# Performance work log

Hardware: AMD Instinct MI355X
Metric: run time of the kernel (lower is better)

Reference implementation:

```python
import jax, jax.numpy as jnp
import numpy as np
import math

N, E = 10000, 160000
MUL0, MUL1 = 64, 32        # node irreps: 64x0e + 32x1o (dim 160)
M0, M1 = 32, 16            # msg irreps: 32x0e + 16x1o (dim 80)
H = 8                      # attention heads
NB = 16                    # radial basis size
C0 = M0 + M1               # coupled scalar mul (48)
C1 = M0 + M1 + M1          # coupled vector mul (64)
WNUM = M0 + M1 + M0 + M1 + M1  # uvu tensor-product weight numel (112)
EPS = 1e-5
SCALE = 1.0 / math.sqrt(M0 + M1)  # 1/sqrt(num_irreps of msg)
MDIM = M0 + 3 * M1


def o3_linear(x0, x1, W0, W1):
    # e3nn o3.Linear: mixes multiplicities within each degree l, shared over m,
    # with 1/sqrt(fan_in) path normalization.
    y0 = (x0 @ W0) * (1.0 / math.sqrt(x0.shape[-1]))
    y1 = jnp.einsum('euc,uv->evc', x1, W1) * (1.0 / math.sqrt(x1.shape[-2]))
    return y0, y1


def setup_inputs() -> dict:
    key = jax.random.key(0)
    k = jax.random.split(key, 16)
    node = jax.random.normal(k[0], (N, MUL0 + 3 * MUL1), jnp.float32)
    rbf = jax.random.normal(k[1], (E, NB), jnp.float32)
    d = jax.random.normal(k[2], (E, 3), jnp.float32)
    d = d / jnp.linalg.norm(d, axis=-1, keepdims=True)
    # component-normalized real spherical harmonics up to l=1: [1, sqrt(3)*r_hat]
    rsh = jnp.concatenate([jnp.ones((E, 1), jnp.float32), math.sqrt(3.0) * d], axis=-1)
    edge_index = jax.random.randint(k[3], (2, E), 0, N, dtype=jnp.int32)
    w = lambda i, shape: jax.random.normal(k[i], shape, jnp.float32)
    return dict(
        node=node, rbf=rbf, rsh=rsh, edge_index=edge_index,
        gamma0=jnp.ones((MUL0,), jnp.float32), gamma1=jnp.ones((MUL1,), jnp.float32),
        Wq0=w(4, (MUL0, H * M0)), Wq1=w(5, (MUL1, H * M1)),
        Wsrc0=w(6, (MUL0, M0)), Wsrc1=w(7, (MUL1, M1)),
        Wdst0=w(8, (MUL0, M0)), Wdst1=w(9, (MUL1, M1)),
        W_rbf=w(10, (NB, WNUM)),
        Wkv0=w(11, (C0, 2 * H * M0)), Wkv1=w(12, (C1, 2 * H * M1)),
        Wmsg0=w(13, (H * M0, MUL0)), Wmsg1=w(14, (H * M1, MUL1)),
    )


def reference(node, rbf, rsh, edge_index, gamma0, gamma1, Wq0, Wq1, Wsrc0, Wsrc1,
              Wdst0, Wdst1, W_rbf, Wkv0, Wkv1, Wmsg0, Wmsg1):
    n = node.shape[0]
    src_i, dst_i = edge_index[0], edge_index[1]
    n0 = node[:, :MUL0]
    n1 = node[:, MUL0:].reshape(n, MUL1, 3)
    # --- equivariant layer norm: standard LN on scalars, RMS-of-norms on vectors ---
    mu = n0.mean(-1, keepdims=True)
    var = ((n0 - mu) ** 2).mean(-1, keepdims=True)
    h0 = (n0 - mu) / jnp.sqrt(var + EPS) * gamma0
    vn = (n1 ** 2).sum(-1).mean(-1, keepdims=True)          # (n,1)
    h1 = n1 / jnp.sqrt(vn + EPS)[..., None] * gamma1[None, :, None]
    # --- query (per-head msg irreps layout) ---
    q0, q1 = o3_linear(h0, h1, Wq0, Wq1)
    q = jnp.concatenate([q0.reshape(n, H, M0),
                         q1.reshape(n, H, M1, 3).reshape(n, H, 3 * M1)], axis=-1)  # (n,H,MDIM)
    # --- per-edge src/dst features ---
    s0, s1 = o3_linear(h0, h1, Wsrc0, Wsrc1)
    d0, d1 = o3_linear(h0, h1, Wdst0, Wdst1)
    x0 = s0[src_i] + d0[dst_i]            # (E, M0)
    x1 = s1[src_i] + d1[dst_i]            # (E, M1, 3)
    # --- CG tensor product ('uvu', external per-edge weights from rbf) ---
    w = rbf @ W_rbf                       # (E, WNUM)
    o = np.cumsum([0, M0, M1, M0, M1, M1])
    w000 = w[:, o[0]:o[1]]; w110 = w[:, o[1]:o[2]]
    w011 = w[:, o[2]:o[3]]; w101 = w[:, o[3]:o[4]]; w111 = w[:, o[4]:o[5]]
    y0 = rsh[:, :1]                       # l=0 sh
    y1 = rsh[:, 1:]                       # l=1 sh
    c0a = w000 * x0 * y0                                                  # 0x0->0
    c0b = w110 * (x1 * y1[:, None, :]).sum(-1) * (1.0 / math.sqrt(3.0))   # 1x1->0
    c1a = w011[..., None] * x0[..., None] * y1[:, None, :]                # 0x1->1
    c1b = w101[..., None] * x1 * y0[..., None]                            # 1x0->1
    c1c = w111[..., None] * jnp.cross(x1, y1[:, None, :]) * (1.0 / math.sqrt(2.0))  # 1x1->1
    cp0 = jnp.concatenate([c0a, c0b], axis=-1)        # (E, C0)
    cp1 = jnp.concatenate([c1a, c1b, c1c], axis=1)    # (E, C1, 3)
    # --- key / value ---
    kv0, kv1 = o3_linear(cp0, cp1, Wkv0, Wkv1)
    kv = jnp.concatenate([kv0.reshape(-1, 2 * H, M0),
                          kv1.reshape(-1, 2 * H, M1, 3).reshape(-1, 2 * H, 3 * M1)], axis=-1)
    kkey, val = kv[:, :H], kv[:, H:]      # (E,H,MDIM) each
    # --- segment softmax over destination nodes (torch_geometric.utils.softmax) ---
    logits = (q[src_i] * kkey).sum(-1, keepdims=True) * SCALE   # (E,H,1)
    smax = jax.ops.segment_max(logits, dst_i, num_segments=n)
    a = jnp.exp(logits - smax[dst_i])
    z = jax.ops.segment_sum(a, dst_i, num_segments=n)
    attn = a / (z[dst_i] + 1e-16)
    # --- scatter-add aggregation ---
    msg = jax.ops.segment_sum(attn * val, dst_i, num_segments=n)  # (n,H,MDIM)
    m0 = msg[:, :, :M0].reshape(n, H * M0)
    m1 = msg[:, :, M0:].reshape(n, H, M1, 3).reshape(n, H * M1, 3)
    o0, o1 = o3_linear(m0, m1, Wmsg0, Wmsg1)
    return node + jnp.concatenate([o0, o1.reshape(n, 3 * MUL1)], axis=-1)
```

## Files before the change

### kernel.cpp

```cpp
#include <hip/hip_runtime.h>
#include <math.h>


constexpr float EPSV        = 1e-5f;
constexpr float INV_SQRT3   = 0.5773502691896258f;
constexpr float INV_SQRT2   = 0.7071067811865476f;
constexpr float INV_SQRT32  = 0.17677669529663687f;
constexpr float INV_SQRT48  = 0.14433756729740643f;
constexpr float INV_SQRT128 = 0.08838834764831845f;
constexpr float SCALE_ATT   = 0.14433756729740643f;

#define LDS_FENCE() do { asm volatile("s_waitcnt lgkmcnt(0)" ::: "memory"); \
                         __builtin_amdgcn_sched_barrier(0); } while (0)

__device__ __forceinline__ float wsum64(float v) {
#pragma unroll
  for (int m = 1; m < 64; m <<= 1) v += __shfl_xor(v, m);
  return v;
}

__device__ __forceinline__ unsigned bf16r(float f) {
  unsigned b = __float_as_uint(f);
  return (b + 0x7FFFu + ((b >> 16) & 1u)) >> 16;
}

__global__ void init_count(unsigned* __restrict__ count, unsigned* __restrict__ count2,
                           int N) {
  int i = blockIdx.x * blockDim.x + threadIdx.x;
  if (i < N) { count[i] = 0u; count2[i] = 0u; }
}

__global__ void k_hist(const int* __restrict__ edge_index,
                       unsigned* __restrict__ count_dst,
                       unsigned* __restrict__ count_src, int E) {
  int e = blockIdx.x * blockDim.x + threadIdx.x;
  if (e < E) {
    atomicAdd(&count_dst[edge_index[(size_t)E + e]], 1u);
    atomicAdd(&count_src[edge_index[e]], 1u);
  }
}

__global__ __launch_bounds__(1024) void k_scan2(
    const unsigned* __restrict__ c0, unsigned* __restrict__ o0, unsigned* __restrict__ u0,
    const unsigned* __restrict__ c1, unsigned* __restrict__ o1, unsigned* __restrict__ u1,
    int N) {
  const unsigned* count = blockIdx.x ? c1 : c0;
  unsigned* offs   = blockIdx.x ? o1 : o0;
  unsigned* cursor = blockIdx.x ? u1 : u0;
  __shared__ unsigned buf[1024];
  __shared__ unsigned carry;
  if (threadIdx.x == 0) carry = 0u;
  __syncthreads();
  for (int base = 0; base < N; base += 1024) {
    int i = base + threadIdx.x;
    unsigned v = (i < N) ? count[i] : 0u;
    buf[threadIdx.x] = v;
    __syncthreads();
    for (int off = 1; off < 1024; off <<= 1) {
      unsigned t = (threadIdx.x >= (unsigned)off) ? buf[threadIdx.x - off] : 0u;
      __syncthreads();
      buf[threadIdx.x] += t;
      __syncthreads();
    }
    unsigned excl = buf[threadIdx.x] - v + carry;
    if (i < N) { offs[i] = excl; cursor[i] = excl; }
    __syncthreads();
    if (threadIdx.x == 1023) carry += buf[1023];
    __syncthreads();
  }
  if (threadIdx.x == 0) offs[N] = carry;
}

__global__ void k_scatter(const int* __restrict__ edge_index,
                          unsigned* __restrict__ cursor, unsigned* __restrict__ sorted,
                          unsigned* __restrict__ cursor2, unsigned* __restrict__ sorted2,
                          int E) {
  int e = blockIdx.x * blockDim.x + threadIdx.x;
  if (e < E) {
    unsigned p0 = atomicAdd(&cursor[edge_index[(size_t)E + e]], 1u);
    sorted[p0] = (unsigned)e;
    unsigned p1 = atomicAdd(&cursor2[edge_index[e]], 1u);
    sorted2[p1] = (unsigned)e;
  }
}

__global__ __launch_bounds__(256) void k_wfold(
    const float* __restrict__ Wq0, const float* __restrict__ Wq1,
    const float* __restrict__ Wkv0, const float* __restrict__ Wkv1,
    unsigned* __restrict__ WATp, unsigned* __restrict__ WBTp) {
  int idx = blockIdx.x * 256 + threadIdx.x;
  if (idx < 32 * 384) {
    int k2 = idx / 384, o = idx % 384;
    int h = o / 48, j = o % 48;
    const float* wq0 = Wq0 + (size_t)(2 * k2) * 256 + h * 32;
    const float* wq1 = Wq0 + (size_t)(2 * k2 + 1) * 256 + h * 32;
    const float* wk  = Wkv0 + (size_t)j * 512 + h * 32;
    float s0 = 0.f, s1 = 0.f;
#pragma unroll
    for (int m = 0; m < 32; m++) { s0 += wq0[m] * wk[m]; s1 += wq1[m] * wk[m]; }
    s0 *= 0.125f * INV_SQRT48; s1 *= 0.125f * INV_SQRT48;
    WATp[idx] = bf16r(s0) | (bf16r(s1) << 16);
  }
  idx -= 32 * 384;
  if (idx >= 0 && idx < 16 * 512) {
    int u2 = idx / 512, o2 = idx % 512;
    int h = o2 / 64, u = o2 % 64;
    const float* wa = Wq1 + (size_t)(2 * u2) * 128 + h * 16;
    const float* wb = Wq1 + (size_t)(2 * u2 + 1) * 128 + h * 16;
    const float* wk = Wkv1 + (size_t)u * 256 + h * 16;
    float s0 = 0.f, s1 = 0.f;
#pragma unroll
    for (int t = 0; t < 16; t++) { s0 += wa[t] * wk[t]; s1 += wb[t] * wk[t]; }
    s0 *= 0.125f * INV_SQRT32; s1 *= 0.125f * INV_SQRT32;
    WBTp[idx] = bf16r(s0) | (bf16r(s1) << 16);
  }
}

__global__ __launch_bounds__(256) void k_node(
    const float* __restrict__ node, const float* __restrict__ gamma0,
    const float* __restrict__ gamma1,
    const unsigned* __restrict__ WATp, const unsigned* __restrict__ WBTp,
    const float* __restrict__ Wsrc0, const float* __restrict__ Wsrc1,
    const float* __restrict__ Wdst0, const float* __restrict__ Wdst1,
    float* __restrict__ qkbuf, float* __restrict__ sbuf, float* __restrict__ dbuf,
    int N) {
  __shared__ unsigned WATL[32 * 384];
  __shared__ unsigned WBTL[16 * 512];
  __shared__ float    hL[16][160];
  __shared__ float    Wsd0L[64 * 64];
  __shared__ float    Wsd1L[32 * 32];

  int t = threadIdx.x;
  for (int i = t; i < 32 * 384; i += 256) WATL[i] = WATp[i];
  for (int i = t; i < 16 * 512; i += 256) WBTL[i] = WBTp[i];
  for (int i = t; i < 64 * 64; i += 256) {
    int k = i >> 6, o3 = i & 63, wh = o3 >> 5, j = o3 & 31;
    Wsd0L[i] = (wh ? Wdst0 : Wsrc0)[k * 32 + j];
  }
  for (int i = t; i < 32 * 32; i += 256) {
    int u = i >> 5, o4 = i & 31, wh = o4 >> 4, v = o4 & 15;
    Wsd1L[i] = (wh ? Wdst1 : Wsrc1)[u * 16 + v];
  }

  int wid = t >> 6, lane = t & 63;
  int n0 = blockIdx.x * 16;
  int nmax = min(16, N - n0);
  if (nmax <= 0) return;

  for (int nl = wid * 4; nl < min(wid * 4 + 4, nmax); nl++) {
    const float* nrow = node + (size_t)(n0 + nl) * 160;
    float v0 = nrow[lane];
    float mu = wsum64(v0) * (1.0f / 64.0f);
    float dv = v0 - mu;
    float var = wsum64(dv * dv) * (1.0f / 64.0f);
    float rs0 = rsqrtf(var + EPSV);
    float a = nrow[64 + lane];
    float b = (lane < 32) ? nrow[128 + lane] : 0.0f;
    float vn = wsum64(a * a + b * b) * (1.0f / 32.0f);
    float rs1 = rsqrtf(vn + EPSV);
    hL[nl][lane] = dv * rs0 * gamma0[lane];
    hL[nl][64 + lane] = a * rs1 * gamma1[lane / 3];
    if (lane < 32) hL[nl][128 + lane] = b * rs1 * gamma1[(64 + lane) / 3];
  }
  __syncthreads();

  int hh = lane & 7, rr = lane >> 3;
  int i0 = t >> 6;
  for (int s = 0; s < 8; s++) {
    int i = i0 + 4 * s;
    if (i >= 30) break;
    int J = rr * 30 + i;
    float acc[16];
#pragma unroll
    for (int n = 0; n < 16; n++) acc[n] = 0.f;
    if (J < 48) {
      int o = hh * 48 + J;
#pragma unroll 2
      for (int k2 = 0; k2 < 32; k2++) {
        unsigned pr = WATL[k2 * 384 + o];
        float w0 = __uint_as_float(pr << 16);
        float w1 = __uint_as_float(pr & 0xFFFF0000u);
#pragma unroll
        for (int n = 0; n < 16; n++) {
          float2 hp = *reinterpret_cast<const float2*>(&hL[n][2 * k2]);
          acc[n] += hp.x * w0 + hp.y * w1;
        }
      }
    } else {
      int u = (J - 48) / 3, c = (J - 48) - 3 * u;
      int o2 = hh * 64 + u;
#pragma unroll 2
      for (int u2 = 0; u2 < 16; u2++) {
        unsigned pr = WBTL[u2 * 512 + o2];
        float w0 = __uint_as_float(pr << 16);
        float w1 = __uint_as_float(pr & 0xFFFF0000u);
#pragma unroll
        for (int n = 0; n < 16; n++)
          acc[n] += hL[n][64 + (2 * u2) * 3 + c] * w0 +
                    hL[n][64 + (2 * u2 + 1) * 3 + c] * w1;
      }
    }
    for (int n = 0; n < nmax; n++)
      qkbuf[(size_t)(n0 + n) * 1920 + i * 64 + lane] = acc[n];
  }

  if (t < 64) {
    int wh = t >> 5, j = t & 31;
    float acc[16];
#pragma unroll
    for (int n = 0; n < 16; n++) acc[n] = 0.f;
    for (int k = 0; k < 64; k++) {
      float w = Wsd0L[k * 64 + t];
#pragma unroll
      for (int n = 0; n < 16; n++) acc[n] += hL[n][k] * w;
    }
    float* obuf = wh ? dbuf : sbuf;
    for (int n = 0; n < nmax; n++) obuf[(size_t)(n0 + n) * 80 + j] = acc[n] * 0.125f;
  } else if (t < 160) {
    int idx = t - 64;
    int wh = idx / 48, vc = idx % 48, v = vc / 3, c = vc - 3 * v;
    float acc[16];
#pragma unroll
    for (int n = 0; n < 16; n++) acc[n] = 0.f;
    for (int u = 0; u < 32; u++) {
      float w = Wsd1L[u * 32 + wh * 16 + v];
#pragma unroll
      for (int n = 0; n < 16; n++) acc[n] += hL[n][64 + u * 3 + c] * w;
    }
    float* obuf = wh ? dbuf : sbuf;
    for (int n = 0; n < nmax; n++)
      obuf[(size_t)(n0 + n) * 80 + 32 + vc] = acc[n] * INV_SQRT32;
  }
}

__device__ __forceinline__ void cp_own_build(
    int u, float xa, float xb, float xc, float wA, float wB,
    float y0, float ya, float yb, float yc,
    float& cp0, float& c0, float& c1, float& c2) {
  if (u < 32) {
    float t0 = wA * xa; cp0 = t0 * y0;
    float t1 = wB * xa; c0 = t1 * ya; c1 = t1 * yb; c2 = t1 * yc;
  } else if (u < 48) {
    float dv = xa * ya + xb * yb + xc * yc;
    cp0 = wA * dv * INV_SQRT3;
    float t1 = wB * y0; c0 = t1 * xa; c1 = t1 * xb; c2 = t1 * xc;
  } else {
    cp0 = 0.f;
    float t1 = wB * INV_SQRT2;
    c0 = t1 * (xb * yc - xc * yb);
    c1 = t1 * (xc * ya - xa * yc);
    c2 = t1 * (xa * yb - xb * ya);
  }
}

__global__ __launch_bounds__(256) void k_logit(
    const float* __restrict__ rbf, const float* __restrict__ rsh,
    const int* __restrict__ edge_index,
    const float* __restrict__ W_rbf,
    const float* __restrict__ qkbuf, const float* __restrict__ sbuf,
    const float* __restrict__ dbuf,
    const unsigned* __restrict__ offs2, const unsigned* __restrict__ sorted2,
    float* __restrict__ logits, int N, int E) {
  int tid = threadIdx.x, wid = tid >> 6, lane = tid & 63;
  int u = lane;
  bool cls0 = (u < 32);
  int tx = cls0 ? 0 : ((u < 48) ? u - 32 : u - 48);
  int idxA = cls0 ? u : 32 + 3 * tx;
  int idxB = cls0 ? u : idxA + 1;
  int idxC = cls0 ? u : idxA + 2;
  int colA = (u < 48) ? u : 48 + u;
  int colB = 48 + u;
  float wcA[16], wcB[16];
#pragma unroll
  for (int k = 0; k < 16; k++) {
    wcA[k] = W_rbf[k * 112 + colA];
    wcB[k] = W_rbf[k * 112 + colB];
  }
  int J1 = 48 + 3 * u, J2 = J1 + 1, J3 = J1 + 2;
  int o0 = (u < 48) ? ((u % 30) * 64 + (u / 30) * 8) : 0;
  int o1 = (J1 % 30) * 64 + (J1 / 30) * 8;
  int o2 = (J2 % 30) * 64 + (J2 / 30) * 8;
  int o3 = (J3 % 30) * 64 + (J3 / 30) * 8;

  int n = blockIdx.x * 4 + wid;
  if (n >= N) return;
  unsigned off = offs2[n];
  int deg = (int)(offs2[n + 1] - off);
  if (deg == 0) return;

  const float* qkr = qkbuf + (size_t)n * 1920;
  float qk0[8], qk1[8], qk2[8], qk3[8];
  if (u < 48) {
    float4 a = *(const float4*)(qkr + o0);
    float4 b = *(const float4*)(qkr + o0 + 4);
    qk0[0]=a.x; qk0[1]=a.y; qk0[2]=a.z; qk0[3]=a.w;
    qk0[4]=b.x; qk0[5]=b.y; qk0[6]=b.z; qk0[7]=b.w;
  } else {
#pragma unroll
    for (int h = 0; h < 8; h++) qk0[h] = 0.f;
  }
  {
    float4 a = *(const float4*)(qkr + o1);
    float4 b = *(const float4*)(qkr + o1 + 4);
    qk1[0]=a.x; qk1[1]=a.y; qk1[2]=a.z; qk1[3]=a.w;
    qk1[4]=b.x; qk1[5]=b.y; qk1[6]=b.z; qk1[7]=b.w;
  }
  {
    float4 a = *(const float4*)(qkr + o2);
    float4 b = *(const float4*)(qkr + o2 + 4);
    qk2[0]=a.x; qk2[1]=a.y; qk2[2]=a.z; qk2[3]=a.w;
    qk2[4]=b.x; qk2[5]=b.y; qk2[6]=b.z; qk2[7]=b.w;
  }
  {
    float4 a = *(const float4*)(qkr + o3);
    float4 b = *(const float4*)(qkr + o3 + 4);
    qk3[0]=a.x; qk3[1]=a.y; qk3[2]=a.z; qk3[3]=a.w;
    qk3[4]=b.x; qk3[5]=b.y; qk3[6]=b.z; qk3[7]=b.w;
  }
  float s0 = sbuf[(size_t)n * 80 + idxA];
  float s1 = sbuf[(size_t)n * 80 + idxB];
  float s2 = sbuf[(size_t)n * 80 + idxC];

  int b0 = lane & 1, b1 = (lane >> 1) & 1, b2 = (lane >> 2) & 1;

  for (int t = 0; t < deg; t++) {
    unsigned e = sorted2[off + t];
    int dst = edge_index[(size_t)E + e];
    const float* drow = dbuf + (size_t)dst * 80;
    float xa = s0 + drow[idxA];
    float xb = s1 + drow[idxB];
    float xc = s2 + drow[idxC];
    const float* rr = rbf + (size_t)e * 16;
    float4 r0 = *(const float4*)(rr);
    float4 r1 = *(const float4*)(rr + 4);
    float4 r2 = *(const float4*)(rr + 8);
    float4 r3 = *(const float4*)(rr + 12);
    float4 y  = *(const float4*)(rsh + (size_t)e * 4);
    float wA = r0.x*wcA[0]+r0.y*wcA[1]+r0.z*wcA[2]+r0.w*wcA[3]
             + r1.x*wcA[4]+r1.y*wcA[5]+r1.z*wcA[6]+r1.w*wcA[7]
             + r2.x*wcA[8]+r2.y*wcA[9]+r2.z*wcA[10]+r2.w*wcA[11]
             + r3.x*wcA[12]+r3.y*wcA[13]+r3.z*wcA[14]+r3.w*wcA[15];
    float wB = r0.x*wcB[0]+r0.y*wcB[1]+r0.z*wcB[2]+r0.w*wcB[3]
             + r1.x*wcB[4]+r1.y*wcB[5]+r1.z*wcB[6]+r1.w*wcB[7]
             + r2.x*wcB[8]+r2.y*wcB[9]+r2.z*wcB[10]+r2.w*wcB[11]
             + r3.x*wcB[12]+r3.y*wcB[13]+r3.z*wcB[14]+r3.w*wcB[15];
    float cp0, c0, c1, c2;
    cp_own_build(u, xa, xb, xc, wA, wB, y.x, y.y, y.z, y.w, cp0, c0, c1, c2);

    float p[8];
#pragma unroll
    for (int h = 0; h < 8; h++)
      p[h] = qk0[h]*cp0 + qk1[h]*c0 + qk2[h]*c1 + qk3[h]*c2;
    float q4[4];
#pragma unroll
    for (int i = 0; i < 4; i++) {
      float mine = b0 ? p[2*i+1] : p[2*i];
      float send = b0 ? p[2*i]   : p[2*i+1];
      q4[i] = mine + __shfl_xor(send, 1);
    }
    float q2a, q2b;
    {
      float mine = b1 ? q4[1] : q4[0];
      float send = b1 ? q4[0] : q4[1];
      q2a = mine + __shfl_xor(send, 2);
      mine = b1 ? q4[3] : q4[2];
      send = b1 ? q4[2] : q4[3];
      q2b = mine + __shfl_xor(send, 2);
    }
    float mine = b2 ? q2b : q2a;
    float send = b2 ? q2a : q2b;
    float q1 = mine + __shfl_xor(send, 4);
    q1 += __shfl_xor(q1, 8);
    q1 += __shfl_xor(q1, 16);
    q1 += __shfl_xor(q1, 32);
    if (lane < 8) logits[(size_t)e * 8 + lane] = q1 * SCALE_ATT;
  }
}

__global__ __launch_bounds__(256) void k_max(
    const float* __restrict__ logits,
    const unsigned* __restrict__ offs, const unsigned* __restrict__ sorted,
    float* __restrict__ mxbuf, int N) {
  int tid = threadIdx.x, wid = tid >> 6, lane = tid & 63;
  int n = blockIdx.x * 4 + wid;
  if (n >= N) return;
  unsigned off = offs[n];
  int deg = (int)(offs[n + 1] - off);
  float mx = -3.4e38f;
  for (int i = lane; i < deg * 8; i += 64) {
    unsigned e = sorted[off + (i >> 3)];
    mx = fmaxf(mx, logits[(size_t)e * 8 + (i & 7)]);
  }
  mx = fmaxf(mx, __shfl_xor(mx, 8));
  mx = fmaxf(mx, __shfl_xor(mx, 16));
  mx = fmaxf(mx, __shfl_xor(mx, 32));
  if (lane < 8) mxbuf[(size_t)n * 8 + lane] = mx;
}

__global__ __launch_bounds__(256, 4) void k_agg(
    const float* __restrict__ rbf, const float* __restrict__ rsh,
    const int* __restrict__ edge_index,
    const float* __restrict__ W_rbf, const float* __restrict__ Wkv0,
    const float* __restrict__ Wkv1,
    const float* __restrict__ sbuf, const float* __restrict__ dbuf,
    const float* __restrict__ logits, const float* __restrict__ mxbuf,
    const unsigned* __restrict__ offs, const unsigned* __restrict__ sorted,
    float* __restrict__ mlbuf, int N, int E) {
  __shared__ float S[4 * 1952];
  int tid = threadIdx.x, wid = tid >> 6, lane = tid & 63;
  float* acpL = S + wid * 1952;
  int u = lane;
  bool cls0 = (u < 32);
  int tx = cls0 ? 0 : ((u < 48) ? u - 32 : u - 48);
  int idxA = cls0 ? u : 32 + 3 * tx;
  int idxB = cls0 ? u : idxA + 1;
  int idxC = cls0 ? u : idxA + 2;
  int colA = (u < 48) ? u : 48 + u;
  int colB = 48 + u;
  float wcA[16], wcB[16];
#pragma unroll
  for (int k = 0; k < 16; k++) {
    wcA[k] = W_rbf[k * 112 + colA];
    wcB[k] = W_rbf[k * 112 + colB];
  }

  int n = blockIdx.x * 4 + wid;
  if (n >= N) return;
  unsigned off = offs[n];
  int deg = (int)(offs[n + 1] - off);
  float* mlrow = mlbuf + (size_t)n * 640;
  if (deg == 0) {
#pragma unroll
    for (int g = 0; g < 10; g++) mlrow[g * 64 + lane] = 0.f;
    return;
  }

  float d0 = dbuf[(size_t)n * 80 + idxA];
  float d1 = dbuf[(size_t)n * 80 + idxB];
  float d2 = dbuf[(size_t)n * 80 + idxC];
  float4 mxa = *(const float4*)(mxbuf + (size_t)n * 8);
  float4 mxb = *(const float4*)(mxbuf + (size_t)n * 8 + 4);

  float acc0[8], acc1[8], acc2[8], acc3[8];
#pragma unroll
  for (int h = 0; h < 8; h++) { acc0[h]=0.f; acc1[h]=0.f; acc2[h]=0.f; acc3[h]=0.f; }
  float z_own = 0.f;

  for (int t = 0; t < deg; t++) {
    unsigned e = sorted[off + t];
    int src = edge_index[e];
    const float* srow = sbuf + (size_t)src * 80;
    float xa = srow[idxA] + d0;
    float xb = srow[idxB] + d1;
    float xc = srow[idxC] + d2;
    const float* rr = rbf + (size_t)e * 16;
    float4 r0 = *(const float4*)(rr);
    float4 r1 = *(const float4*)(rr + 4);
    float4 r2 = *(const float4*)(rr + 8);
    float4 r3 = *(const float4*)(rr + 12);
    float4 y  = *(const float4*)(rsh + (size_t)e * 4);
    float wA = r0.x*wcA[0]+r0.y*wcA[1]+r0.z*wcA[2]+r0.w*wcA[3]
             + r1.x*wcA[4]+r1.y*wcA[5]+r1.z*wcA[6]+r1.w*wcA[7]
             + r2.x*wcA[8]+r2.y*wcA[9]+r2.z*wcA[10]+r2.w*wcA[11]
             + r3.x*wcA[12]+r3.y*wcA[13]+r3.z*wcA[14]+r3.w*wcA[15];
    float wB = r0.x*wcB[0]+r0.y*wcB[1]+r0.z*wcB[2]+r0.w*wcB[3]
             + r1.x*wcB[4]+r1.y*wcB[5]+r1.z*wcB[6]+r1.w*wcB[7]
             + r2.x*wcB[8]+r2.y*wcB[9]+r2.z*wcB[10]+r2.w*wcB[11]
             + r3.x*wcB[12]+r3.y*wcB[13]+r3.z*wcB[14]+r3.w*wcB[15];
    float cp0, c0, c1, c2;
    cp_own_build(u, xa, xb, xc, wA, wB, y.x, y.y, y.z, y.w, cp0, c0, c1, c2);

    float4 lgA = *(const float4*)(logits + (size_t)e * 8);
    float4 lgB = *(const float4*)(logits + (size_t)e * 8 + 4);
    float aa[8];
    aa[0] = __expf(lgA.x - mxa.x); aa[1] = __expf(lgA.y - mxa.y);
    aa[2] = __expf(lgA.z - mxa.z); aa[3] = __expf(lgA.w - mxa.w);
    aa[4] = __expf(lgB.x - mxb.x); aa[5] = __expf(lgB.y - mxb.y);
    aa[6] = __expf(lgB.z - mxb.z); aa[7] = __expf(lgB.w - mxb.w);
    float aaz = (u & 4) ? ((u & 2) ? ((u & 1) ? aa[7] : aa[6])
                                   : ((u & 1) ? aa[5] : aa[4]))
                        : ((u & 2) ? ((u & 1) ? aa[3] : aa[2])
                                   : ((u & 1) ? aa[1] : aa[0]));
    z_own += aaz;
#pragma unroll
    for (int h = 0; h < 8; h++) {
      acc0[h] += aa[h] * cp0;
      acc1[h] += aa[h] * c0;
      acc2[h] += aa[h] * c1;
      acc3[h] += aa[h] * c2;
    }
  }

  int base = 48 + 3 * u;
#pragma unroll
  for (int h = 0; h < 8; h++) {
    if (u < 48) acpL[h * 241 + u] = acc0[h];
    acpL[h * 241 + base + 0] = acc1[h];
    acpL[h * 241 + base + 1] = acc2[h];
    acpL[h * 241 + base + 2] = acc3[h];
  }
  LDS_FENCE();

#pragma unroll
  for (int g = 0; g < 4; g++) {
    int col = g * 64 + lane;
    int h2 = col >> 5;
    float a2 = 0.f;
#pragma unroll
    for (int k = 0; k < 48; k++) a2 += acpL[h2 * 241 + k] * Wkv0[k * 512 + 256 + col];
    float zz = __shfl(z_own, h2);
    mlrow[col] = a2 * INV_SQRT48 / (zz + 1e-16f);
  }
#pragma unroll
  for (int g = 0; g < 6; g++) {
    int pc = g * 64 + lane;
    int p = pc / 3, c = pc - p * 3;
    int h2 = p >> 4;
    float a2 = 0.f;
#pragma unroll
    for (int w = 0; w < 64; w++)
      a2 += acpL[h2 * 241 + 48 + w * 3 + c] * Wkv1[w * 256 + 128 + p];
    float zz = __shfl(z_own, h2);
    mlrow[256 + pc] = a2 * 0.125f / (zz + 1e-16f);
  }
}

__global__ __launch_bounds__(256) void k_out(
    const float* __restrict__ node, const float* __restrict__ mlbuf,
    const float* __restrict__ Wmsg0, const float* __restrict__ Wmsg1,
    float* __restrict__ out, int N) {
  __shared__ float mlw[4][640];
  int tid = threadIdx.x, wid = tid >> 6, lane = tid & 63;
  int n = blockIdx.x * 4 + wid;
  if (n >= N) return;
  const float* mlrow = mlbuf + (size_t)n * 640;
#pragma unroll
  for (int g = 0; g < 10; g++) mlw[wid][g * 64 + lane] = mlrow[g * 64 + lane];
  LDS_FENCE();
  const float* nrow = node + (size_t)n * 160;
  float* orow = out + (size_t)n * 160;
  {
    float a2 = 0.f;
#pragma unroll 8
    for (int j = 0; j < 256; j++) a2 += mlw[wid][j] * Wmsg0[j * 64 + lane];
    orow[lane] = nrow[lane] + a2 * 0.0625f;
  }
#pragma unroll
  for (int i0 = 0; i0 < 96; i0 += 64) {
    int i = i0 + lane;
    if (i < 96) {
      int v = i / 3, c = i - v * 3;
      float a2 = 0.f;
#pragma unroll 8
      for (int p = 0; p < 128; p++) a2 += mlw[wid][256 + p * 3 + c] * Wmsg1[p * 32 + v];
      orow[64 + i] = nrow[64 + i] + a2 * INV_SQRT128;
    }
  }
}

extern "C" void kernel_launch(void* const* d_in, const int* in_sizes, int n_in,
                              void* d_out, int out_size, void* d_ws, size_t ws_size,
                              hipStream_t stream) {
  (void)n_in; (void)out_size; (void)ws_size;
  const float* node   = (const float*)d_in[0];
  const float* rbf    = (const float*)d_in[1];
  const float* rsh    = (const float*)d_in[2];
  const int*   eidx   = (const int*)d_in[3];
  const float* gamma0 = (const float*)d_in[4];
  const float* gamma1 = (const float*)d_in[5];
  const float* Wq0    = (const float*)d_in[6];
  const float* Wq1    = (const float*)d_in[7];
  const float* Wsrc0  = (const float*)d_in[8];
  const float* Wsrc1  = (const float*)d_in[9];
  const float* Wdst0  = (const float*)d_in[10];
  const float* Wdst1  = (const float*)d_in[11];
  const float* W_rbf  = (const float*)d_in[12];
  const float* Wkv0   = (const float*)d_in[13];
  const float* Wkv1   = (const float*)d_in[14];
  const float* Wmsg0  = (const float*)d_in[15];
  const float* Wmsg1  = (const float*)d_in[16];
  float* out = (float*)d_out;

  int N = in_sizes[0] / 160;
  int E = in_sizes[3] / 2;

  unsigned* WATp = (unsigned*)d_ws;
  unsigned* WBTp = WATp + 32 * 384;
  float* sbuf   = (float*)(WBTp + 16 * 512);
  float* dbuf   = sbuf + (size_t)N * 80;
  float* qkbuf  = dbuf + (size_t)N * 80;
  float* mlbuf  = qkbuf + (size_t)N * 1920;
  float* logits = mlbuf + (size_t)N * 640;
  float* mxbuf  = logits + (size_t)E * 8;
  unsigned* count   = (unsigned*)(mxbuf + (size_t)N * 8);
  unsigned* offs    = count + N;
  unsigned* cursor  = offs + N + 1;
  unsigned* sorted  = cursor + N;
  unsigned* count2  = sorted + E;
  unsigned* offs2   = count2 + N;
  unsigned* cursor2 = offs2 + N + 1;
  unsigned* sorted2 = cursor2 + N;

  hipLaunchKernelGGL(init_count, dim3((N + 255) / 256), dim3(256), 0, stream,
                     count, count2, N);
  hipLaunchKernelGGL(k_hist, dim3((E + 255) / 256), dim3(256), 0, stream,
                     eidx, count, count2, E);
  hipLaunchKernelGGL(k_scan2, dim3(2), dim3(1024), 0, stream,
                     count, offs, cursor, count2, offs2, cursor2, N);
  hipLaunchKernelGGL(k_scatter, dim3((E + 255) / 256), dim3(256), 0, stream,
                     eidx, cursor, sorted, cursor2, sorted2, E);
  hipLaunchKernelGGL(k_wfold, dim3(80), dim3(256), 0, stream,
                     Wq0, Wq1, Wkv0, Wkv1, WATp, WBTp);
  hipLaunchKernelGGL(k_node, dim3((N + 15) / 16), dim3(256), 0, stream,
                     node, gamma0, gamma1, WATp, WBTp, Wsrc0, Wsrc1, Wdst0, Wdst1,
                     qkbuf, sbuf, dbuf, N);
  hipLaunchKernelGGL(k_logit, dim3((N + 3) / 4), dim3(256), 0, stream,
                     rbf, rsh, eidx, W_rbf, qkbuf, sbuf, dbuf,
                     offs2, sorted2, logits, N, E);
  hipLaunchKernelGGL(k_max, dim3((N + 3) / 4), dim3(256), 0, stream,
                     logits, offs, sorted, mxbuf, N);
  hipLaunchKernelGGL(k_agg, dim3((N + 3) / 4), dim3(256), 0, stream,
                     rbf, rsh, eidx, W_rbf, Wkv0, Wkv1, sbuf, dbuf, logits, mxbuf,
                     offs, sorted, mlbuf, N, E);
  hipLaunchKernelGGL(k_out, dim3((N + 3) / 4), dim3(256), 0, stream,
                     node, mlbuf, Wmsg0, Wmsg1, out, N);
}
```

Before: 734.6 us.

## Split node kernel into norm and qk kernels with per-lane weight layout

The fused k_node kernel, which staged about 80KB of folded weights in LDS per 16-node block, is split in two. k_norm does the layer norm and the src/dst projections one node per wave and writes the normalized features to a scratch buffer. k_qk reads the packed bf16 weights straight from global or cache, with the folded weights reordered so that consecutive lanes read consecutive words. The qkbuf layout is changed to match, and k_logit's offsets are updated. This removes the large per-block LDS fill and the occupancy cap it imposed, at the cost of an extra kernel launch and a round trip of the normalized features through global memory.

```diff
diff --git a/kernel.cpp b/kernel.cpp
--- a/kernel.cpp
+++ b/kernel.cpp
@@ -84,27 +84,27 @@
   }
 }
 
-__global__ __launch_bounds__(256) void k_wfold(
+__global__ __launch_bounds__(256) void k_wfold2(
     const float* __restrict__ Wq0, const float* __restrict__ Wq1,
     const float* __restrict__ Wkv0, const float* __restrict__ Wkv1,
-    unsigned* __restrict__ WATp, unsigned* __restrict__ WBTp) {
+    unsigned* __restrict__ WS, unsigned* __restrict__ WV) {
   int idx = blockIdx.x * 256 + threadIdx.x;
   if (idx < 32 * 384) {
-    int k2 = idx / 384, o = idx % 384;
-    int h = o / 48, j = o % 48;
+    int k2 = idx / 384, oq = idx % 384;
+    int J = oq >> 3, h = oq & 7;
     const float* wq0 = Wq0 + (size_t)(2 * k2) * 256 + h * 32;
     const float* wq1 = Wq0 + (size_t)(2 * k2 + 1) * 256 + h * 32;
-    const float* wk  = Wkv0 + (size_t)j * 512 + h * 32;
+    const float* wk  = Wkv0 + (size_t)J * 512 + h * 32;
     float s0 = 0.f, s1 = 0.f;
 #pragma unroll
     for (int m = 0; m < 32; m++) { s0 += wq0[m] * wk[m]; s1 += wq1[m] * wk[m]; }
     s0 *= 0.125f * INV_SQRT48; s1 *= 0.125f * INV_SQRT48;
-    WATp[idx] = bf16r(s0) | (bf16r(s1) << 16);
+    WS[idx] = bf16r(s0) | (bf16r(s1) << 16);
   }
   idx -= 32 * 384;
   if (idx >= 0 && idx < 16 * 512) {
-    int u2 = idx / 512, o2 = idx % 512;
-    int h = o2 / 64, u = o2 % 64;
+    int u2 = idx / 512, uh = idx % 512;
+    int u = uh >> 3, h = uh & 7;
     const float* wa = Wq1 + (size_t)(2 * u2) * 128 + h * 16;
     const float* wb = Wq1 + (size_t)(2 * u2 + 1) * 128 + h * 16;
     const float* wk = Wkv1 + (size_t)u * 256 + h * 16;
@@ -112,124 +112,140 @@
 #pragma unroll
     for (int t = 0; t < 16; t++) { s0 += wa[t] * wk[t]; s1 += wb[t] * wk[t]; }
     s0 *= 0.125f * INV_SQRT32; s1 *= 0.125f * INV_SQRT32;
-    WBTp[idx] = bf16r(s0) | (bf16r(s1) << 16);
-  }
-}
-
-__global__ __launch_bounds__(256) void k_node(
+    WV[idx] = bf16r(s0) | (bf16r(s1) << 16);
+  }
+}
+
+__global__ __launch_bounds__(256) void k_norm(
     const float* __restrict__ node, const float* __restrict__ gamma0,
     const float* __restrict__ gamma1,
-    const unsigned* __restrict__ WATp, const unsigned* __restrict__ WBTp,
     const float* __restrict__ Wsrc0, const float* __restrict__ Wsrc1,
     const float* __restrict__ Wdst0, const float* __restrict__ Wdst1,
-    float* __restrict__ qkbuf, float* __restrict__ sbuf, float* __restrict__ dbuf,
+    float* __restrict__ hbuf, float* __restrict__ sbuf, float* __restrict__ dbuf,
     int N) {
-  __shared__ unsigned WATL[32 * 384];
-  __shared__ unsigned WBTL[16 * 512];
-  __shared__ float    hL[16][160];
-  __shared__ float    Wsd0L[64 * 64];
-  __shared__ float    Wsd1L[32 * 32];
-
-  int t = threadIdx.x;
-  for (int i = t; i < 32 * 384; i += 256) WATL[i] = WATp[i];
-  for (int i = t; i < 16 * 512; i += 256) WBTL[i] = WBTp[i];
-  for (int i = t; i < 64 * 64; i += 256) {
-    int k = i >> 6, o3 = i & 63, wh = o3 >> 5, j = o3 & 31;
-    Wsd0L[i] = (wh ? Wdst0 : Wsrc0)[k * 32 + j];
-  }
-  for (int i = t; i < 32 * 32; i += 256) {
-    int u = i >> 5, o4 = i & 31, wh = o4 >> 4, v = o4 & 15;
-    Wsd1L[i] = (wh ? Wdst1 : Wsrc1)[u * 16 + v];
-  }
-
-  int wid = t >> 6, lane = t & 63;
-  int n0 = blockIdx.x * 16;
-  int nmax = min(16, N - n0);
-  if (nmax <= 0) return;
-
-  for (int nl = wid * 4; nl < min(wid * 4 + 4, nmax); nl++) {
-    const float* nrow = node + (size_t)(n0 + nl) * 160;
-    float v0 = nrow[lane];
-    float mu = wsum64(v0) * (1.0f / 64.0f);
-    float dv = v0 - mu;
-    float var = wsum64(dv * dv) * (1.0f / 64.0f);
-    float rs0 = rsqrtf(var + EPSV);
-    float a = nrow[64 + lane];
-    float b = (lane < 32) ? nrow[128 + lane] : 0.0f;
-    float vn = wsum64(a * a + b * b) * (1.0f / 32.0f);
-    float rs1 = rsqrtf(vn + EPSV);
-    hL[nl][lane] = dv * rs0 * gamma0[lane];
-    hL[nl][64 + lane] = a * rs1 * gamma1[lane / 3];
-    if (lane < 32) hL[nl][128 + lane] = b * rs1 * gamma1[(64 + lane) / 3];
+  __shared__ float hL[4][160];
+  int tid = threadIdx.x, wid = tid >> 6, lane = tid & 63;
+  int n = blockIdx.x * 4 + wid;
+  if (n >= N) return;
+  float* h = hL[wid];
+  const float* nrow = node + (size_t)n * 160;
+
+  float v0 = nrow[lane];
+  float mu = wsum64(v0) * (1.0f / 64.0f);
+  float dv = v0 - mu;
+  float var = wsum64(dv * dv) * (1.0f / 64.0f);
+  float rs0 = rsqrtf(var + EPSV);
+  float a = nrow[64 + lane];
+  float b = (lane < 32) ? nrow[128 + lane] : 0.0f;
+  float vn = wsum64(a * a + b * b) * (1.0f / 32.0f);
+  float rs1 = rsqrtf(vn + EPSV);
+  h[lane] = dv * rs0 * gamma0[lane];
+  h[64 + lane] = a * rs1 * gamma1[lane / 3];
+  if (lane < 32) h[128 + lane] = b * rs1 * gamma1[(64 + lane) / 3];
+  LDS_FENCE();
+
+  float* hrow = hbuf + (size_t)n * 160;
+  hrow[lane] = h[lane];
+  hrow[64 + lane] = h[64 + lane];
+  if (lane < 32) hrow[128 + lane] = h[128 + lane];
+
+  {
+    int wh = lane >> 5, j = lane & 31;
+    const float* W0 = wh ? Wdst0 : Wsrc0;
+    float acc = 0.f;
+#pragma unroll
+    for (int k = 0; k < 64; k++) acc += h[k] * W0[k * 32 + j];
+    (wh ? dbuf : sbuf)[(size_t)n * 80 + j] = acc * 0.125f;
+  }
+#pragma unroll
+  for (int i0 = 0; i0 < 96; i0 += 64) {
+    int i = i0 + lane;
+    if (i < 96) {
+      int wh = i / 48, vc = i % 48, v = vc / 3, cc = vc - 3 * v;
+      const float* W1 = wh ? Wdst1 : Wsrc1;
+      float acc = 0.f;
+#pragma unroll
+      for (int u = 0; u < 32; u++) acc += h[64 + u * 3 + cc] * W1[u * 16 + v];
+      (wh ? dbuf : sbuf)[(size_t)n * 80 + 32 + vc] = acc * INV_SQRT32;
+    }
+  }
+}
+
+__global__ __launch_bounds__(256) void k_qk(
+    const float* __restrict__ hbuf,
+    const unsigned* __restrict__ WS, const unsigned* __restrict__ WV,
+    float* __restrict__ qkbuf, int N) {
+  __shared__ float hsL[8 * 64];
+  __shared__ float hoV[8 * 96];
+  int tid = threadIdx.x, wid = tid >> 6, lane = tid & 63;
+  int n0 = blockIdx.x * 8;
+  int nn = min(8, N - n0);
+  if (nn <= 0) return;
+
+  for (int idx = tid; idx < 512; idx += 256) {
+    int n = idx >> 6, k = idx & 63;
+    hsL[idx] = (n < nn) ? hbuf[(size_t)(n0 + n) * 160 + k] : 0.f;
+  }
+  for (int idx = tid; idx < 768; idx += 256) {
+    int n = idx / 96, r = idx % 96, u2 = r / 6, q = r % 6, c = q >> 1, j = q & 1;
+    hoV[idx] = (n < nn) ? hbuf[(size_t)(n0 + n) * 160 + 64 + (2 * u2 + j) * 3 + c] : 0.f;
   }
   __syncthreads();
 
-  int hh = lane & 7, rr = lane >> 3;
-  int i0 = t >> 6;
-  for (int s = 0; s < 8; s++) {
-    int i = i0 + 4 * s;
-    if (i >= 30) break;
-    int J = rr * 30 + i;
-    float acc[16];
-#pragma unroll
-    for (int n = 0; n < 16; n++) acc[n] = 0.f;
-    if (J < 48) {
-      int o = hh * 48 + J;
-#pragma unroll 2
-      for (int k2 = 0; k2 < 32; k2++) {
-        unsigned pr = WATL[k2 * 384 + o];
+  if (wid == 0) {
+    float acc[6][8];
+#pragma unroll
+    for (int g = 0; g < 6; g++)
+#pragma unroll
+      for (int n = 0; n < 8; n++) acc[g][n] = 0.f;
+    for (int k2 = 0; k2 < 32; ++k2) {
+      float2 hp[8];
+#pragma unroll
+      for (int n = 0; n < 8; n++)
+        hp[n] = *reinterpret_cast<const float2*>(&hsL[n * 64 + 2 * k2]);
+#pragma unroll
+      for (int g = 0; g < 6; g++) {
+        unsigned pr = WS[k2 * 384 + g * 64 + lane];
         float w0 = __uint_as_float(pr << 16);
         float w1 = __uint_as_float(pr & 0xFFFF0000u);
 #pragma unroll
-        for (int n = 0; n < 16; n++) {
-          float2 hp = *reinterpret_cast<const float2*>(&hL[n][2 * k2]);
-          acc[n] += hp.x * w0 + hp.y * w1;
-        }
+        for (int n = 0; n < 8; n++) acc[g][n] += hp[n].x * w0 + hp[n].y * w1;
       }
-    } else {
-      int u = (J - 48) / 3, c = (J - 48) - 3 * u;
-      int o2 = hh * 64 + u;
-#pragma unroll 2
-      for (int u2 = 0; u2 < 16; u2++) {
-        unsigned pr = WBTL[u2 * 512 + o2];
+    }
+#pragma unroll
+    for (int g = 0; g < 6; g++)
+      for (int n = 0; n < nn; n++)
+        qkbuf[(size_t)(n0 + n) * 1920 + g * 64 + lane] = acc[g][n];
+  } else {
+    int c = wid - 1;
+    float acc[8][8];
+#pragma unroll
+    for (int g = 0; g < 8; g++)
+#pragma unroll
+      for (int n = 0; n < 8; n++) acc[g][n] = 0.f;
+    for (int u2 = 0; u2 < 16; ++u2) {
+      float2 hv[8];
+#pragma unroll
+      for (int n = 0; n < 8; n++)
+        hv[n] = *reinterpret_cast<const float2*>(&hoV[n * 96 + u2 * 6 + 2 * c]);
+#pragma unroll
+      for (int g = 0; g < 8; g++) {
+        unsigned pr = WV[u2 * 512 + g * 64 + lane];
         float w0 = __uint_as_float(pr << 16);
         float w1 = __uint_as_float(pr & 0xFFFF0000u);
 #pragma unroll
-        for (int n = 0; n < 16; n++)
-          acc[n] += hL[n][64 + (2 * u2) * 3 + c] * w0 +
-                    hL[n][64 + (2 * u2 + 1) * 3 + c] * w1;
+        for (int n = 0; n < 8; n++) acc[g][n] += hv[n].x * w0 + hv[n].y * w1;
       }
     }
-    for (int n = 0; n < nmax; n++)
-      qkbuf[(size_t)(n0 + n) * 1920 + i * 64 + lane] = acc[n];
-  }
-
-  if (t < 64) {
-    int wh = t >> 5, j = t & 31;
-    float acc[16];
-#pragma unroll
-    for (int n = 0; n < 16; n++) acc[n] = 0.f;
-    for (int k = 0; k < 64; k++) {
-      float w = Wsd0L[k * 64 + t];
-#pragma unroll
-      for (int n = 0; n < 16; n++) acc[n] += hL[n][k] * w;
-    }
-    float* obuf = wh ? dbuf : sbuf;
-    for (int n = 0; n < nmax; n++) obuf[(size_t)(n0 + n) * 80 + j] = acc[n] * 0.125f;
-  } else if (t < 160) {
-    int idx = t - 64;
-    int wh = idx / 48, vc = idx % 48, v = vc / 3, c = vc - 3 * v;
-    float acc[16];
-#pragma unroll
-    for (int n = 0; n < 16; n++) acc[n] = 0.f;
-    for (int u = 0; u < 32; u++) {
-      float w = Wsd1L[u * 32 + wh * 16 + v];
-#pragma unroll
-      for (int n = 0; n < 16; n++) acc[n] += hL[n][64 + u * 3 + c] * w;
-    }
-    float* obuf = wh ? dbuf : sbuf;
-    for (int n = 0; n < nmax; n++)
-      obuf[(size_t)(n0 + n) * 80 + 32 + vc] = acc[n] * INV_SQRT32;
+    int u = 0, h = lane & 7;
+#pragma unroll
+    for (int g = 0; g < 8; g++) {
+      int uh = g * 64 + lane;
+      u = uh >> 3;
+      int p = 384 + u * 24 + c * 8 + h;
+      for (int n = 0; n < nn; n++)
+        qkbuf[(size_t)(n0 + n) * 1920 + p] = acc[g][n];
+    }
   }
 }
 
@@ -276,11 +292,10 @@
     wcA[k] = W_rbf[k * 112 + colA];
     wcB[k] = W_rbf[k * 112 + colB];
   }
-  int J1 = 48 + 3 * u, J2 = J1 + 1, J3 = J1 + 2;
-  int o0 = (u < 48) ? ((u % 30) * 64 + (u / 30) * 8) : 0;
-  int o1 = (J1 % 30) * 64 + (J1 / 30) * 8;
-  int o2 = (J2 % 30) * 64 + (J2 / 30) * 8;
-  int o3 = (J3 % 30) * 64 + (J3 / 30) * 8;
+  int o0 = (u < 48) ? (u * 8) : 0;
+  int o1 = 384 + u * 24;
+  int o2 = o1 + 8;
+  int o3 = o1 + 16;
 
   int n = blockIdx.x * 4 + wid;
   if (n >= N) return;
@@ -584,12 +599,13 @@
   int N = in_sizes[0] / 160;
   int E = in_sizes[3] / 2;
 
-  unsigned* WATp = (unsigned*)d_ws;
-  unsigned* WBTp = WATp + 32 * 384;
-  float* sbuf   = (float*)(WBTp + 16 * 512);
+  unsigned* WS  = (unsigned*)d_ws;
+  unsigned* WV  = WS + 12288;
+  float* sbuf   = (float*)(WV + 8192);
   float* dbuf   = sbuf + (size_t)N * 80;
   float* qkbuf  = dbuf + (size_t)N * 80;
   float* mlbuf  = qkbuf + (size_t)N * 1920;
+  float* hbuf   = mlbuf;
   float* logits = mlbuf + (size_t)N * 640;
   float* mxbuf  = logits + (size_t)E * 8;
   unsigned* count   = (unsigned*)(mxbuf + (size_t)N * 8);
@@ -609,11 +625,13 @@
                      count, offs, cursor, count2, offs2, cursor2, N);
   hipLaunchKernelGGL(k_scatter, dim3((E + 255) / 256), dim3(256), 0, stream,
                      eidx, cursor, sorted, cursor2, sorted2, E);
-  hipLaunchKernelGGL(k_wfold, dim3(80), dim3(256), 0, stream,
-                     Wq0, Wq1, Wkv0, Wkv1, WATp, WBTp);
-  hipLaunchKernelGGL(k_node, dim3((N + 15) / 16), dim3(256), 0, stream,
-                     node, gamma0, gamma1, WATp, WBTp, Wsrc0, Wsrc1, Wdst0, Wdst1,
-                     qkbuf, sbuf, dbuf, N);
+  hipLaunchKernelGGL(k_wfold2, dim3(80), dim3(256), 0, stream,
+                     Wq0, Wq1, Wkv0, Wkv1, WS, WV);
+  hipLaunchKernelGGL(k_norm, dim3((N + 3) / 4), dim3(256), 0, stream,
+                     node, gamma0, gamma1, Wsrc0, Wsrc1, Wdst0, Wdst1,
+                     hbuf, sbuf, dbuf, N);
+  hipLaunchKernelGGL(k_qk, dim3((N + 7) / 8), dim3(256), 0, stream,
+                     hbuf, WS, WV, qkbuf, N);
   hipLaunchKernelGGL(k_logit, dim3((N + 3) / 4), dim3(256), 0, stream,
                      rbf, rsh, eidx, W_rbf, qkbuf, sbuf, dbuf,
                      offs2, sorted2, logits, N, E);
```

Measured after the change: 602.2 us. 1.22x faster.
